# Kernel optimization log

Hardware: AMD Instinct MI355X
Metric: run time of the kernel (lower is better)

Reference implementation:

```python
import jax, jax.numpy as jnp
import numpy as np

WINDOW_SIZE = 7
CHANNELS = 3
C1 = 0.01 ** 2
C2 = 0.03 ** 2


def _gaussian_window():
    # 1D gaussian, sigma=1.5, normalized; outer product -> 2D window
    coords = jnp.arange(WINDOW_SIZE, dtype=jnp.float32) - WINDOW_SIZE // 2
    g = jnp.exp(-coords ** 2 / (2 * 1.5 ** 2))
    g = g / g.sum()
    w2d = g[:, None] * g[None, :]  # [7,7]
    # depthwise kernel [C,1,7,7] (OIHW with feature_group_count=C)
    return jnp.tile(w2d[None, None], (CHANNELS, 1, 1, 1))


def _dwconv(x, window):
    pad = WINDOW_SIZE // 2
    return jax.lax.conv_general_dilated(
        x, window,
        window_strides=(1, 1),
        padding=[(pad, pad), (pad, pad)],
        dimension_numbers=('NCHW', 'OIHW', 'NCHW'),
        feature_group_count=CHANNELS,
    )


def setup_inputs() -> dict:
    key = jax.random.key(0)
    k1, k2 = jax.random.split(key)
    shape = (16, 3, 512, 512)
    enhanced = jax.random.uniform(k1, shape, dtype=jnp.float32)
    target = jax.random.uniform(k2, shape, dtype=jnp.float32)
    return {"enhanced": enhanced, "target": target}


def reference(enhanced, target):
    window = _gaussian_window()
    mu1 = _dwconv(enhanced, window)
    mu2 = _dwconv(target, window)
    mu1_sq = mu1 ** 2
    mu2_sq = mu2 ** 2
    mu1_mu2 = mu1 * mu2
    sigma1_sq = _dwconv(enhanced ** 2, window) - mu1_sq
    sigma2_sq = _dwconv(target ** 2, window) - mu2_sq
    sigma12 = _dwconv(enhanced * target, window) - mu1_mu2
    ssim_map = ((2 * mu1_mu2 + C1) * (2 * sigma12 + C2)) / (
        (mu1_sq + mu2_sq + C1) * (sigma1_sq + sigma2_sq + C2))
    return 1.0 - ssim_map.mean()
```

## Files before the change

kernel.cpp:

```cpp
#include <hip/hip_runtime.h>


#define TILE_W 64
#define TILE_H 16
#define HALO 3
#define IN_H 22
#define H_PAIRS 66
#define IMG_H 512
#define IMG_W 512
#define NPLANES 48
#define SSIM_C1 1.0e-4f
#define SSIM_C2 9.0e-4f

static __device__ constexpr float G[7] = {
    0.03663284536f, 0.11128076166f, 0.21674531251f, 0.27068216094f,
    0.21674531251f, 0.11128076166f, 0.03663284536f};

__device__ __forceinline__ float4 ld4z(const float* __restrict__ row, int col) {
  if (col >= 0 && col + 3 < IMG_W) {
    return *reinterpret_cast<const float4*>(row + col);
  }
  float4 v;
  v.x = ((unsigned)(col + 0) < IMG_W) ? row[col + 0] : 0.f;
  v.y = ((unsigned)(col + 1) < IMG_W) ? row[col + 1] : 0.f;
  v.z = ((unsigned)(col + 2) < IMG_W) ? row[col + 2] : 0.f;
  v.w = ((unsigned)(col + 3) < IMG_W) ? row[col + 3] : 0.f;
  return v;
}

__global__ __launch_bounds__(256, 6) void ssim_tile_kernel(
    const float* __restrict__ x, const float* __restrict__ y,
    float* __restrict__ partial) {
  __shared__ __align__(16) float2 hbuf[2][IN_H][H_PAIRS];

  const int tid = threadIdx.x;
  const int plane = blockIdx.z;
  const float* __restrict__ xp = x + (size_t)plane * (IMG_H * IMG_W);
  const float* __restrict__ yp = y + (size_t)plane * (IMG_H * IMG_W);
  const int y0 = blockIdx.y * TILE_H - HALO;
  const int cbase = blockIdx.x * TILE_W - 4;
  const bool edge = (blockIdx.x == 0) | (blockIdx.x == gridDim.x - 1) |
                    (blockIdx.y == 0) | (blockIdx.y == gridDim.y - 1);

  for (int item = tid; item < IN_H * 16; item += 256) {
    const int hr = item >> 4;
    const int cg = item & 15;
    const int bcol = cbase + 4 * cg;
    float xin[12], yin[12];
    if (!edge) {
      const float* xr = xp + (size_t)(y0 + hr) * IMG_W + bcol;
      const float* yr = yp + (size_t)(y0 + hr) * IMG_W + bcol;
      const float4 xa = *reinterpret_cast<const float4*>(xr);
      const float4 xb = *reinterpret_cast<const float4*>(xr + 4);
      const float4 xc = *reinterpret_cast<const float4*>(xr + 8);
      const float4 ya = *reinterpret_cast<const float4*>(yr);
      const float4 yb = *reinterpret_cast<const float4*>(yr + 4);
      const float4 yc = *reinterpret_cast<const float4*>(yr + 8);
      xin[0] = xa.x; xin[1] = xa.y; xin[2] = xa.z; xin[3] = xa.w;
      xin[4] = xb.x; xin[5] = xb.y; xin[6] = xb.z; xin[7] = xb.w;
      xin[8] = xc.x; xin[9] = xc.y; xin[10] = xc.z; xin[11] = xc.w;
      yin[0] = ya.x; yin[1] = ya.y; yin[2] = ya.z; yin[3] = ya.w;
      yin[4] = yb.x; yin[5] = yb.y; yin[6] = yb.z; yin[7] = yb.w;
      yin[8] = yc.x; yin[9] = yc.y; yin[10] = yc.z; yin[11] = yc.w;
    } else {
      const int gy = y0 + hr;
      if ((unsigned)gy < IMG_H) {
        const float* xr = xp + (size_t)gy * IMG_W;
        const float* yr = yp + (size_t)gy * IMG_W;
#pragma unroll
        for (int v = 0; v < 3; ++v) {
          const float4 a = ld4z(xr, bcol + 4 * v);
          const float4 b = ld4z(yr, bcol + 4 * v);
          xin[4 * v + 0] = a.x; xin[4 * v + 1] = a.y;
          xin[4 * v + 2] = a.z; xin[4 * v + 3] = a.w;
          yin[4 * v + 0] = b.x; yin[4 * v + 1] = b.y;
          yin[4 * v + 2] = b.z; yin[4 * v + 3] = b.w;
        }
      } else {
#pragma unroll
        for (int i = 0; i < 12; ++i) { xin[i] = 0.f; yin[i] = 0.f; }
      }
    }
    float a1[4] = {0.f, 0.f, 0.f, 0.f};
    float a2[4] = {0.f, 0.f, 0.f, 0.f};
    float aS[4] = {0.f, 0.f, 0.f, 0.f};
    float aXY[4] = {0.f, 0.f, 0.f, 0.f};
#pragma unroll
    for (int w = 1; w < 12; ++w) {
      const float xv = xin[w];
      const float yv = yin[w];
      const float ps = fmaf(xv, xv, yv * yv);
      const float pxy = xv * yv;
#pragma unroll
      for (int j = 0; j < 4; ++j) {
        const int k = w - 1 - j;
        if (k >= 0 && k < 7) {
          const float gk = G[k];
          a1[j] = fmaf(gk, xv, a1[j]);
          a2[j] = fmaf(gk, yv, a2[j]);
          aS[j] = fmaf(gk, ps, aS[j]);
          aXY[j] = fmaf(gk, pxy, aXY[j]);
        }
      }
    }
    float2* b0 = &hbuf[0][hr][4 * cg];
    float2* b1 = &hbuf[1][hr][4 * cg];
#pragma unroll
    for (int j = 0; j < 4; ++j) {
      b0[j] = make_float2(a1[j], a2[j]);
      b1[j] = make_float2(aS[j], aXY[j]);
    }
  }
  __syncthreads();

  const int c = tid & 63;
  const int r0 = (tid >> 6) * 4;
  float m1[4] = {0.f, 0.f, 0.f, 0.f};
  float m2[4] = {0.f, 0.f, 0.f, 0.f};
  float eS[4] = {0.f, 0.f, 0.f, 0.f};
  float eXY[4] = {0.f, 0.f, 0.f, 0.f};
#pragma unroll
  for (int j = 0; j < 10; ++j) {
    const float2 mv = hbuf[0][r0 + j][c];
    const float2 sv = hbuf[1][r0 + j][c];
#pragma unroll
    for (int t = 0; t < 4; ++t) {
      const int k = j - t;
      if (k >= 0 && k < 7) {
        const float gk = G[k];
        m1[t] = fmaf(gk, mv.x, m1[t]);
        m2[t] = fmaf(gk, mv.y, m2[t]);
        eS[t] = fmaf(gk, sv.x, eS[t]);
        eXY[t] = fmaf(gk, sv.y, eXY[t]);
      }
    }
  }

  float acc = 0.f;
#pragma unroll
  for (int t = 0; t < 4; ++t) {
    const float mu12 = m1[t] * m2[t];
    const float msq = fmaf(m1[t], m1[t], m2[t] * m2[t]);
    const float sig12 = eXY[t] - mu12;
    const float sigsum = eS[t] - msq;
    const float num = fmaf(2.f, mu12, SSIM_C1) * fmaf(2.f, sig12, SSIM_C2);
    const float den = (msq + SSIM_C1) * (sigsum + SSIM_C2);
    float r = __builtin_amdgcn_rcpf(den);
    r = r * fmaf(-den, r, 2.f);
    acc = fmaf(num, r, acc);
  }

#pragma unroll
  for (int off = 32; off > 0; off >>= 1) acc += __shfl_down(acc, off, 64);
  __shared__ float wsum[4];
  if ((tid & 63) == 0) wsum[tid >> 6] = acc;
  __syncthreads();
  if (tid == 0) {
    const float s = wsum[0] + wsum[1] + wsum[2] + wsum[3];
    partial[(size_t)blockIdx.z * gridDim.x * gridDim.y +
            (size_t)blockIdx.y * gridDim.x + blockIdx.x] = s;
  }
}

__global__ __launch_bounds__(256) void ssim_reduce_kernel(
    const float* __restrict__ partial, int n, float* __restrict__ out) {
  float acc = 0.f;
  const int nv = n >> 2;
  const float4* __restrict__ p4 = reinterpret_cast<const float4*>(partial);
  for (int i = threadIdx.x; i < nv; i += 256) {
    const float4 v = p4[i];
    acc += (v.x + v.y) + (v.z + v.w);
  }
#pragma unroll
  for (int off = 32; off > 0; off >>= 1) acc += __shfl_down(acc, off, 64);
  __shared__ float wsum[4];
  if ((threadIdx.x & 63) == 0) wsum[threadIdx.x >> 6] = acc;
  __syncthreads();
  if (threadIdx.x == 0) {
    const float s = wsum[0] + wsum[1] + wsum[2] + wsum[3];
    out[0] = 1.f - s * (1.f / (float)(NPLANES * IMG_H * IMG_W));
  }
}

extern "C" void kernel_launch(void* const* d_in, const int* in_sizes, int n_in,
                              void* d_out, int out_size, void* d_ws, size_t ws_size,
                              hipStream_t stream) {
  const float* enhanced = (const float*)d_in[0];
  const float* target = (const float*)d_in[1];
  float* out = (float*)d_out;
  float* partial = (float*)d_ws;

  dim3 grid(IMG_W / TILE_W, IMG_H / TILE_H, NPLANES);
  dim3 block(256, 1, 1);
  ssim_tile_kernel<<<grid, block, 0, stream>>>(enhanced, target, partial);

  const int nblocks = (IMG_W / TILE_W) * (IMG_H / TILE_H) * NPLANES;
  ssim_reduce_kernel<<<1, 256, 0, stream>>>(partial, nblocks, out);
}
```

Measured before the change: 162.3 us.

## Use packed FP32 FMA and wider 8-column horizontal work per thread

Replaces scalar FMAs in both horizontal and vertical Gaussian passes with inline-asm v_pk_fma_f32 on float2 pairs, halving FMA instruction count. Each horizontal-pass thread now produces 8 outputs from a 16-wide window instead of 4 from 12, which cuts redundant loads and taps but leaves only 176 of 256 threads active in that phase. The shared buffer row is padded to 67 float2 to change bank mapping, and the final reduce kernel runs 1024 threads. Risks include lower parallelism in the first phase and higher register pressure under the 6-block launch bound.

Result: faster. 158.2 us (-2.5%).

```diff
diff --git a/kernel.cpp b/kernel.cpp
--- a/kernel.cpp
+++ b/kernel.cpp
@@ -5,7 +5,7 @@
 #define TILE_H 16
 #define HALO 3
 #define IN_H 22
-#define H_PAIRS 66
+#define H_PAIRS 67
 #define IMG_H 512
 #define IMG_W 512
 #define NPLANES 48
@@ -15,6 +15,13 @@
 static __device__ constexpr float G[7] = {
     0.03663284536f, 0.11128076166f, 0.21674531251f, 0.27068216094f,
     0.21674531251f, 0.11128076166f, 0.03663284536f};
+
+__device__ __forceinline__ float2 pk_fma(const float2 a, const float2 b,
+                                         const float2 c) {
+  float2 d;
+  asm("v_pk_fma_f32 %0, %1, %2, %3" : "=v"(d) : "v"(a), "v"(b), "v"(c));
+  return d;
+}
 
 __device__ __forceinline__ float4 ld4z(const float* __restrict__ row, int col) {
   if (col >= 0 && col + 3 < IMG_W) {
@@ -38,87 +45,84 @@
   const float* __restrict__ xp = x + (size_t)plane * (IMG_H * IMG_W);
   const float* __restrict__ yp = y + (size_t)plane * (IMG_H * IMG_W);
   const int y0 = blockIdx.y * TILE_H - HALO;
-  const int cbase = blockIdx.x * TILE_W - 4;
+  const int x0 = blockIdx.x * TILE_W;
   const bool edge = (blockIdx.x == 0) | (blockIdx.x == gridDim.x - 1) |
                     (blockIdx.y == 0) | (blockIdx.y == gridDim.y - 1);
 
-  for (int item = tid; item < IN_H * 16; item += 256) {
-    const int hr = item >> 4;
-    const int cg = item & 15;
-    const int bcol = cbase + 4 * cg;
-    float xin[12], yin[12];
+  if (tid < IN_H * 8) {
+    const int hr = tid >> 3;
+    const int cg = tid & 7;
+    const int bcol = x0 + 8 * cg - 4;
+    float wx[16], wy[16];
+    const int gy = y0 + hr;
     if (!edge) {
-      const float* xr = xp + (size_t)(y0 + hr) * IMG_W + bcol;
-      const float* yr = yp + (size_t)(y0 + hr) * IMG_W + bcol;
-      const float4 xa = *reinterpret_cast<const float4*>(xr);
-      const float4 xb = *reinterpret_cast<const float4*>(xr + 4);
-      const float4 xc = *reinterpret_cast<const float4*>(xr + 8);
-      const float4 ya = *reinterpret_cast<const float4*>(yr);
-      const float4 yb = *reinterpret_cast<const float4*>(yr + 4);
-      const float4 yc = *reinterpret_cast<const float4*>(yr + 8);
-      xin[0] = xa.x; xin[1] = xa.y; xin[2] = xa.z; xin[3] = xa.w;
-      xin[4] = xb.x; xin[5] = xb.y; xin[6] = xb.z; xin[7] = xb.w;
-      xin[8] = xc.x; xin[9] = xc.y; xin[10] = xc.z; xin[11] = xc.w;
-      yin[0] = ya.x; yin[1] = ya.y; yin[2] = ya.z; yin[3] = ya.w;
-      yin[4] = yb.x; yin[5] = yb.y; yin[6] = yb.z; yin[7] = yb.w;
-      yin[8] = yc.x; yin[9] = yc.y; yin[10] = yc.z; yin[11] = yc.w;
+      const float* xr = xp + (size_t)gy * IMG_W + bcol;
+      const float* yr = yp + (size_t)gy * IMG_W + bcol;
+#pragma unroll
+      for (int v = 0; v < 4; ++v) {
+        const float4 a = *reinterpret_cast<const float4*>(xr + 4 * v);
+        const float4 b = *reinterpret_cast<const float4*>(yr + 4 * v);
+        wx[4 * v + 0] = a.x; wx[4 * v + 1] = a.y;
+        wx[4 * v + 2] = a.z; wx[4 * v + 3] = a.w;
+        wy[4 * v + 0] = b.x; wy[4 * v + 1] = b.y;
+        wy[4 * v + 2] = b.z; wy[4 * v + 3] = b.w;
+      }
+    } else if ((unsigned)gy < IMG_H) {
+      const float* xr = xp + (size_t)gy * IMG_W;
+      const float* yr = yp + (size_t)gy * IMG_W;
+#pragma unroll
+      for (int v = 0; v < 4; ++v) {
+        const float4 a = ld4z(xr, bcol + 4 * v);
+        const float4 b = ld4z(yr, bcol + 4 * v);
+        wx[4 * v + 0] = a.x; wx[4 * v + 1] = a.y;
+        wx[4 * v + 2] = a.z; wx[4 * v + 3] = a.w;
+        wy[4 * v + 0] = b.x; wy[4 * v + 1] = b.y;
+        wy[4 * v + 2] = b.z; wy[4 * v + 3] = b.w;
+      }
     } else {
-      const int gy = y0 + hr;
-      if ((unsigned)gy < IMG_H) {
-        const float* xr = xp + (size_t)gy * IMG_W;
-        const float* yr = yp + (size_t)gy * IMG_W;
-#pragma unroll
-        for (int v = 0; v < 3; ++v) {
-          const float4 a = ld4z(xr, bcol + 4 * v);
-          const float4 b = ld4z(yr, bcol + 4 * v);
-          xin[4 * v + 0] = a.x; xin[4 * v + 1] = a.y;
-          xin[4 * v + 2] = a.z; xin[4 * v + 3] = a.w;
-          yin[4 * v + 0] = b.x; yin[4 * v + 1] = b.y;
-          yin[4 * v + 2] = b.z; yin[4 * v + 3] = b.w;
+#pragma unroll
+      for (int i = 0; i < 16; ++i) { wx[i] = 0.f; wy[i] = 0.f; }
+    }
+    float2 A[8], B[8];
+#pragma unroll
+    for (int j = 0; j < 8; ++j) {
+      A[j] = make_float2(0.f, 0.f);
+      B[j] = make_float2(0.f, 0.f);
+    }
+#pragma unroll
+    for (int wi = 1; wi < 15; ++wi) {
+      const float xv = wx[wi];
+      const float yv = wy[wi];
+      const float2 xyp = make_float2(xv, yv);
+      const float2 spp = make_float2(fmaf(xv, xv, yv * yv), xv * yv);
+#pragma unroll
+      for (int j = 0; j < 8; ++j) {
+        const int k = wi - 1 - j;
+        if (k >= 0 && k < 7) {
+          const float2 gk2 = make_float2(G[k], G[k]);
+          A[j] = pk_fma(gk2, xyp, A[j]);
+          B[j] = pk_fma(gk2, spp, B[j]);
         }
-      } else {
-#pragma unroll
-        for (int i = 0; i < 12; ++i) { xin[i] = 0.f; yin[i] = 0.f; }
-      }
-    }
-    float a1[4] = {0.f, 0.f, 0.f, 0.f};
-    float a2[4] = {0.f, 0.f, 0.f, 0.f};
-    float aS[4] = {0.f, 0.f, 0.f, 0.f};
-    float aXY[4] = {0.f, 0.f, 0.f, 0.f};
-#pragma unroll
-    for (int w = 1; w < 12; ++w) {
-      const float xv = xin[w];
-      const float yv = yin[w];
-      const float ps = fmaf(xv, xv, yv * yv);
-      const float pxy = xv * yv;
-#pragma unroll
-      for (int j = 0; j < 4; ++j) {
-        const int k = w - 1 - j;
-        if (k >= 0 && k < 7) {
-          const float gk = G[k];
-          a1[j] = fmaf(gk, xv, a1[j]);
-          a2[j] = fmaf(gk, yv, a2[j]);
-          aS[j] = fmaf(gk, ps, aS[j]);
-          aXY[j] = fmaf(gk, pxy, aXY[j]);
-        }
-      }
-    }
-    float2* b0 = &hbuf[0][hr][4 * cg];
-    float2* b1 = &hbuf[1][hr][4 * cg];
-#pragma unroll
-    for (int j = 0; j < 4; ++j) {
-      b0[j] = make_float2(a1[j], a2[j]);
-      b1[j] = make_float2(aS[j], aXY[j]);
+      }
+    }
+    float2* b0 = &hbuf[0][hr][8 * cg];
+    float2* b1 = &hbuf[1][hr][8 * cg];
+#pragma unroll
+    for (int j = 0; j < 8; ++j) {
+      b0[j] = A[j];
+      b1[j] = B[j];
     }
   }
   __syncthreads();
 
   const int c = tid & 63;
   const int r0 = (tid >> 6) * 4;
-  float m1[4] = {0.f, 0.f, 0.f, 0.f};
-  float m2[4] = {0.f, 0.f, 0.f, 0.f};
-  float eS[4] = {0.f, 0.f, 0.f, 0.f};
-  float eXY[4] = {0.f, 0.f, 0.f, 0.f};
+  float2 M[4], S4[4];
+#pragma unroll
+  for (int t = 0; t < 4; ++t) {
+    M[t] = make_float2(0.f, 0.f);
+    S4[t] = make_float2(0.f, 0.f);
+  }
 #pragma unroll
   for (int j = 0; j < 10; ++j) {
     const float2 mv = hbuf[0][r0 + j][c];
@@ -127,11 +131,9 @@
     for (int t = 0; t < 4; ++t) {
       const int k = j - t;
       if (k >= 0 && k < 7) {
-        const float gk = G[k];
-        m1[t] = fmaf(gk, mv.x, m1[t]);
-        m2[t] = fmaf(gk, mv.y, m2[t]);
-        eS[t] = fmaf(gk, sv.x, eS[t]);
-        eXY[t] = fmaf(gk, sv.y, eXY[t]);
+        const float2 gk2 = make_float2(G[k], G[k]);
+        M[t] = pk_fma(gk2, mv, M[t]);
+        S4[t] = pk_fma(gk2, sv, S4[t]);
       }
     }
   }
@@ -139,10 +141,12 @@
   float acc = 0.f;
 #pragma unroll
   for (int t = 0; t < 4; ++t) {
-    const float mu12 = m1[t] * m2[t];
-    const float msq = fmaf(m1[t], m1[t], m2[t] * m2[t]);
-    const float sig12 = eXY[t] - mu12;
-    const float sigsum = eS[t] - msq;
+    const float mu1 = M[t].x, mu2 = M[t].y;
+    const float eS = S4[t].x, eXY = S4[t].y;
+    const float mu12 = mu1 * mu2;
+    const float msq = fmaf(mu1, mu1, mu2 * mu2);
+    const float sig12 = eXY - mu12;
+    const float sigsum = eS - msq;
     const float num = fmaf(2.f, mu12, SSIM_C1) * fmaf(2.f, sig12, SSIM_C2);
     const float den = (msq + SSIM_C1) * (sigsum + SSIM_C2);
     float r = __builtin_amdgcn_rcpf(den);
@@ -162,22 +166,24 @@
   }
 }
 
-__global__ __launch_bounds__(256) void ssim_reduce_kernel(
+__global__ __launch_bounds__(1024) void ssim_reduce_kernel(
     const float* __restrict__ partial, int n, float* __restrict__ out) {
   float acc = 0.f;
   const int nv = n >> 2;
   const float4* __restrict__ p4 = reinterpret_cast<const float4*>(partial);
-  for (int i = threadIdx.x; i < nv; i += 256) {
+  for (int i = threadIdx.x; i < nv; i += 1024) {
     const float4 v = p4[i];
     acc += (v.x + v.y) + (v.z + v.w);
   }
 #pragma unroll
   for (int off = 32; off > 0; off >>= 1) acc += __shfl_down(acc, off, 64);
-  __shared__ float wsum[4];
+  __shared__ float wsum[16];
   if ((threadIdx.x & 63) == 0) wsum[threadIdx.x >> 6] = acc;
   __syncthreads();
   if (threadIdx.x == 0) {
-    const float s = wsum[0] + wsum[1] + wsum[2] + wsum[3];
+    float s = 0.f;
+#pragma unroll
+    for (int w = 0; w < 16; ++w) s += wsum[w];
     out[0] = 1.f - s * (1.f / (float)(NPLANES * IMG_H * IMG_W));
   }
 }
@@ -195,5 +201,5 @@
   ssim_tile_kernel<<<grid, block, 0, stream>>>(enhanced, target, partial);
 
   const int nblocks = (IMG_W / TILE_W) * (IMG_H / TILE_H) * NPLANES;
-  ssim_reduce_kernel<<<1, 256, 0, stream>>>(partial, nblocks, out);
-}
+  ssim_reduce_kernel<<<1, 1024, 0, stream>>>(partial, nblocks, out);
+}
```
